# Performance work log

Hardware: AMD Instinct MI355X
Metric: run time of the kernel (lower is better)

Reference implementation:

```python
import jax, jax.numpy as jnp
import numpy as np

B, CIN, COUT = 16, 32, 64
H = W = 64
K = 3                      # kernel side
GRID_SIZE, SPLINE_ORDER = 5, 3
P = K * K                  # in_features of each KANLinear
GR0, GR1 = -1.0, 1.0       # grid_range


def make_grid():
    # torch: grid = arange(-k, G+k+1)*h + grid_range[0], expanded to (in_features, G+2k+1)
    h = (GR1 - GR0) / GRID_SIZE
    g = jnp.arange(-SPLINE_ORDER, GRID_SIZE + SPLINE_ORDER + 1, dtype=jnp.float32) * h + GR0
    return jnp.broadcast_to(g, (P, g.shape[0]))


def b_splines(x, grid):
    # Cox-de Boor recursion. x: (..., P) -> bases: (..., P, GRID_SIZE+SPLINE_ORDER)
    xe = x[..., None]
    bases = ((xe >= grid[:, :-1]) & (xe < grid[:, 1:])).astype(x.dtype)
    for j in range(1, SPLINE_ORDER + 1):
        left = (xe - grid[:, : -(j + 1)]) / (grid[:, j:-1] - grid[:, : -(j + 1)])
        right = (grid[:, j + 1 :] - xe) / (grid[:, j + 1 :] - grid[:, 1:-j])
        bases = left * bases[..., :-1] + right * bases[..., 1:]
    return bases


def setup_inputs() -> dict:
    key = jax.random.key(0)
    k1, k2, k3, k4 = jax.random.split(key, 4)
    x = jax.random.normal(k1, (B, CIN, H, W), dtype=jnp.float32)
    base_weight = jax.random.normal(k2, (COUT, CIN, P), dtype=jnp.float32) * (1.0 / np.sqrt(P))
    spline_weight = jax.random.normal(k3, (COUT, CIN, P, GRID_SIZE + SPLINE_ORDER), dtype=jnp.float32) * 0.1
    spline_scaler = jax.random.normal(k4, (COUT, CIN, P), dtype=jnp.float32) * (1.0 / np.sqrt(P))
    return {"x": x, "base_weight": base_weight, "spline_weight": spline_weight, "spline_scaler": spline_scaler}


def reference(x, base_weight, spline_weight, spline_scaler):
    grid = make_grid()
    # im2col like torch.nn.Unfold: (B, CIN*P, Hout, Wout), channel-major feature order
    patches = jax.lax.conv_general_dilated_patches(x, (K, K), (1, 1), "VALID")
    _, _, Ho, Wo = patches.shape
    patches = patches.reshape(B, CIN, P, Ho * Wo).transpose(0, 1, 3, 2)  # (B, CIN, L, P)
    # base branch: SiLU(x) @ base_weight^T, summed over input channels per output channel
    base_out = jnp.einsum("bclp,ocp->bol", jax.nn.silu(patches), base_weight)
    # spline branch: B-spline bases contracted with scaled spline weights
    bases = b_splines(patches, grid)                       # (B, CIN, L, P, G+k)
    scaled_w = spline_weight * spline_scaler[..., None]    # (COUT, CIN, P, G+k)
    spline_out = jnp.einsum("bclpg,ocpg->bol", bases, scaled_w)
    return (base_out + spline_out).reshape(B, COUT, Ho, Wo)
```

## Files before the change

### kernel.cpp

```cpp
#include <hip/hip_runtime.h>


typedef short v8s __attribute__((ext_vector_type(8)));
typedef float v4f __attribute__((ext_vector_type(4)));
typedef int   v4i __attribute__((ext_vector_type(4)));
typedef int   v8i __attribute__((ext_vector_type(8)));

#define FSPL8_OFF   0u
#define FSILU_OFF   16777472u
#define WMX_OFF     20972032u
#define WF8_OFF     21103104u
#define WPACKS_OFF  21119488u

#define SCALE1 0x7F7F7F7Fu

__device__ __forceinline__ unsigned short f2bf(float f) {
  unsigned int u = __float_as_uint(f);
  u += 0x7fffu + ((u >> 16) & 1u);
  return (unsigned short)(u >> 16);
}

__global__ __launch_bounds__(256) void k_feat(const float* __restrict__ x,
                                              unsigned char* __restrict__ ws) {
  const int bid = blockIdx.x;
  const int b = bid >> 6, y = bid & 63;
  const int t = threadIdx.x;
  const int xx = t & 63, cg = t >> 6;
  unsigned short h[8];
#pragma unroll
  for (int k = 0; k < 8; ++k) {
    const int c = cg * 8 + k;
    const float v = x[(((size_t)(b * 32 + c) * 64 + y) * 64) + xx];
    h[k] = f2bf(v / (1.0f + __expf(-v)));
    float bb[11];
#pragma unroll
    for (int i = 0; i < 11; ++i) {
      float t0 = -2.2f + 0.4f * i;
      bb[i] = (v >= t0 && v < t0 + 0.4f) ? 1.0f : 0.0f;
    }
#pragma unroll
    for (int j = 1; j <= 3; ++j) {
      float rj = 1.0f / (0.4f * j);
#pragma unroll
      for (int i = 0; i + j < 11; ++i) {
        float ti = -2.2f + 0.4f * i;
        bb[i] = (v - ti) * rj * bb[i] + ((ti + 0.4f * (j + 1)) - v) * rj * bb[i + 1];
      }
    }
    uint2 o;
    unsigned w0 = __builtin_amdgcn_cvt_pk_fp8_f32(bb[0], bb[1], 0, false);
    w0 = __builtin_amdgcn_cvt_pk_fp8_f32(bb[2], bb[3], w0, true);
    unsigned w1 = __builtin_amdgcn_cvt_pk_fp8_f32(bb[4], bb[5], 0, false);
    w1 = __builtin_amdgcn_cvt_pk_fp8_f32(bb[6], bb[7], w1, true);
    o.x = w0; o.y = w1;
    *(uint2*)(ws + FSPL8_OFF + ((((size_t)(b * 32 + c) * 64 + y) * 64) + xx) * 8) = o;
  }
  uint4 s;
  s.x = (unsigned)h[0] | ((unsigned)h[1] << 16);
  s.y = (unsigned)h[2] | ((unsigned)h[3] << 16);
  s.z = (unsigned)h[4] | ((unsigned)h[5] << 16);
  s.w = (unsigned)h[6] | ((unsigned)h[7] << 16);
  *(uint4*)(ws + FSILU_OFF + (size_t)(b * 4096 + y * 64 + xx) * 64 + cg * 16) = s;
}

__global__ __launch_bounds__(256) void k_wpack(const float* __restrict__ bw,
                                               const float* __restrict__ sw,
                                               const float* __restrict__ sc,
                                               unsigned char* __restrict__ ws) {
  int tid = blockIdx.x * 256 + threadIdx.x;
  if (tid >= 165888) return;
  if (tid < 147456) {
    int k, dst;
    if (tid < 131072) {
      int bh = tid & 15, lane = (tid >> 4) & 63, pc = (tid >> 10) & 1;
      int ss = (tid >> 13) & 1, p = tid >> 14;
      k = p * 288 + ss * 128 + (lane >> 4) * 32 + pc * 16 + bh;
      dst = WMX_OFF + tid;
    } else {
      int t2 = tid - 131072;
      int e = t2 & 7, lane = (t2 >> 3) & 63, p = t2 >> 11;
      k = p * 288 + 256 + (lane >> 4) * 8 + e;
      dst = WF8_OFF + t2;
    }
    int ot = (tid < 131072) ? ((tid >> 11) & 3) : (((tid - 131072) >> 9) & 3);
    int lane = (tid < 131072) ? ((tid >> 4) & 63) : (((tid - 131072) >> 3) & 63);
    int o = (ot << 4) + (lane & 15);
    int chunk = k / 24, u = k - chunk * 24;
    int dj = u >> 3, g = u & 7;
    int c = chunk / 3, di = chunk - c * 3;
    int p_tap = di * 3 + dj;
    float val = sw[((size_t)(o * 32 + c) * 9 + p_tap) * 8 + g] *
                sc[(size_t)(o * 32 + c) * 9 + p_tap];
    ws[dst] = (unsigned char)(__builtin_amdgcn_cvt_pk_fp8_f32(val, 0.f, 0, false) & 0xff);
  } else {
    int t2 = tid - 147456;
    int e = t2 & 7, lane = (t2 >> 3) & 63, ot = (t2 >> 9) & 3, sp = t2 >> 11;
    int o = (ot << 4) + (lane & 15);
    int cc = ((lane >> 4) << 3) + e;
    float val = bw[(size_t)(o * 32 + cc) * 9 + sp];
    *(unsigned short*)(ws + WPACKS_OFF + (size_t)t2 * 2) = f2bf(val);
  }
}

__device__ __forceinline__ void ld16(unsigned char* ldsp, const unsigned char* gp) {
  __builtin_amdgcn_global_load_lds(
      (const __attribute__((address_space(1))) unsigned int*)gp,
      (__attribute__((address_space(3))) unsigned int*)ldsp, 16, 0, 0);
}

__global__ __launch_bounds__(512) void k_gemm(const unsigned char* __restrict__ ws,
                                              float* __restrict__ out) {
  __shared__ __align__(16) unsigned char wl8[2][18432];
  __shared__ __align__(16) unsigned char fl8[2][12544];
  __shared__ __align__(16) unsigned char wsil[36864];
  __shared__ __align__(16) unsigned char fsil[25088];

  const int blk = blockIdx.x;
  const int b = blk >> 4, ig = blk & 15;
  const int i0 = ig * 4;
  const int tid = threadIdx.x;
  const int wave = tid >> 6, lane = tid & 63;
  const int q = lane >> 4, ln = lane & 15;
  const int r = wave >> 1, oh = wave & 1;
  const int i = i0 + r;

  auto stage_spl = [&](int p, int bi) {
#pragma unroll
    for (int it = 0; it < 4; ++it) {
      const int u = wave + it * 8;
      if (u < 16) {
        ld16(&wl8[bi][u * 1024], ws + WMX_OFF + (size_t)p * 16384 + (size_t)u * 1024 + lane * 16);
      } else if (u < 18) {
        ld16(&wl8[bi][u * 1024], ws + WF8_OFF + (size_t)p * 2048 + (size_t)(u - 16) * 1024 + lane * 16);
      } else if (u < 30) {
        const int v = u - 18;
        const int cp = v / 3, cr = v - cp * 3;
        ld16(&fl8[bi][v * 1024],
             ws + FSPL8_OFF + ((size_t)((b * 32 + p * 4 + cp) * 64 + i0 + cr * 2)) * 512 + lane * 16);
      }
    }
  };

  auto stage_silu = [&]() {
#pragma unroll
    for (int it = 0; it < 8; ++it) {
      const int u = wave + it * 8;
      if (u < 36) {
        ld16(&wsil[u * 1024], ws + WPACKS_OFF + (size_t)u * 1024 + lane * 16);
      } else if (u < 60) {
        const int v = u - 36;
        const int rr = v >> 2, p4 = v & 3;
        const int y = min(i0 + rr, 63);
        ld16(&fsil[v * 1024],
             ws + FSILU_OFF + (size_t)(b * 64 + y) * 4096 +
                 (p4 * 16 + (lane >> 2)) * 64 + ((lane & 3) ^ ((lane >> 2) & 3)) * 16);
      }
    }
  };

  auto offf = [&](int sg, int qq) {
    int rid = 4 * sg + qq;
    int ch = rid / 3, sub = rid - ch * 3;
    int cp = ch / 3, di = ch - cp * 3;
    return cp * 3072 + (r + di) * 512 + (sub + ln) * 8;
  };
  int offA[4], offB[4];
#pragma unroll
  for (int qq = 0; qq < 4; ++qq) { offA[qq] = offf(q, qq); offB[qq] = offf(4 + q, qq); }
  const int off8 = offf(8, q);

  v4f acc[2][4];
#pragma unroll
  for (int a = 0; a < 2; ++a)
#pragma unroll
    for (int c = 0; c < 4; ++c) acc[a][c] = (v4f){0.f, 0.f, 0.f, 0.f};

  stage_silu();
  stage_spl(0, 0);
  __syncthreads();

#pragma unroll 1
  for (int t = 0; t < 8; ++t) {
    if (t < 7) stage_spl(t + 1, (t + 1) & 1);
    const unsigned char* wb = wl8[t & 1];
    const unsigned char* fb = fl8[t & 1];
#pragma unroll
    for (int ss = 0; ss < 2; ++ss) {
      union { v8i v; v4i h[2]; } wf[2];
#pragma unroll
      for (int tt = 0; tt < 2; ++tt) {
        const unsigned char* wp = wb + ss * 8192 + (oh * 2 + tt) * 2048 + lane * 16;
        wf[tt].h[0] = *(const v4i*)(wp);
        wf[tt].h[1] = *(const v4i*)(wp + 1024);
      }
      const int* offs = ss ? offB : offA;
      union { v8i v; long l[4]; } ff[4];
#pragma unroll
      for (int pt = 0; pt < 4; ++pt)
#pragma unroll
        for (int qq = 0; qq < 4; ++qq)
          ff[pt].l[qq] = *(const long*)(fb + offs[qq] + pt * 128);
#pragma unroll
      for (int tt = 0; tt < 2; ++tt)
#pragma unroll
        for (int pt = 0; pt < 4; ++pt)
          acc[tt][pt] = __builtin_amdgcn_mfma_scale_f32_16x16x128_f8f6f4(
              wf[tt].v, ff[pt].v, acc[tt][pt], 0, 0, 0, SCALE1, 0, SCALE1);
    }
    {
      long w8[2], f8[4];
#pragma unroll
      for (int tt = 0; tt < 2; ++tt)
        w8[tt] = *(const long*)(wb + 16384 + (oh * 2 + tt) * 512 + lane * 8);
#pragma unroll
      for (int pt = 0; pt < 4; ++pt)
        f8[pt] = *(const long*)(fb + off8 + pt * 128);
#pragma unroll
      for (int tt = 0; tt < 2; ++tt)
#pragma unroll
        for (int pt = 0; pt < 4; ++pt)
          acc[tt][pt] = __builtin_amdgcn_mfma_f32_16x16x32_fp8_fp8(
              w8[tt], f8[pt], acc[tt][pt], 0, 0, 0);
    }
    __syncthreads();
  }

#pragma unroll
  for (int e = 0; e < 9; ++e) {
    const int di = e / 3, dj = e % 3;
    v8s wb2[2], fb2[4];
#pragma unroll
    for (int tt = 0; tt < 2; ++tt)
      wb2[tt] = *(const v8s*)(&wsil[0] + e * 4096 + (oh * 2 + tt) * 1024 + lane * 16);
    const int xb = dj + ln;
    const int sbase = (r + di) * 4096 + xb * 64 + ((q ^ (xb & 3)) * 16);
#pragma unroll
    for (int pt = 0; pt < 4; ++pt)
      fb2[pt] = *(const v8s*)(&fsil[0] + sbase + pt * 1024);
#pragma unroll
    for (int tt = 0; tt < 2; ++tt)
#pragma unroll
      for (int pt = 0; pt < 4; ++pt)
        acc[tt][pt] = __builtin_amdgcn_mfma_f32_16x16x32_bf16(
            wb2[tt], fb2[pt], acc[tt][pt], 0, 0, 0);
  }

  if (i < 62) {
#pragma unroll
    for (int tt = 0; tt < 2; ++tt)
#pragma unroll
      for (int pt = 0; pt < 4; ++pt) {
        const int j = pt * 16 + ln;
        if (j < 62) {
#pragma unroll
          for (int rr = 0; rr < 4; ++rr) {
            const int o = (oh * 2 + tt) * 16 + q * 4 + rr;
            out[(((size_t)b * 64 + o) * 62 + i) * 62 + j] = acc[tt][pt][rr];
          }
        }
      }
  }
}

extern "C" void kernel_launch(void* const* d_in, const int* in_sizes, int n_in,
                              void* d_out, int out_size, void* d_ws, size_t ws_size,
                              hipStream_t stream) {
  const float* x  = (const float*)d_in[0];
  const float* bw = (const float*)d_in[1];
  const float* sw = (const float*)d_in[2];
  const float* sc = (const float*)d_in[3];
  unsigned char* ws = (unsigned char*)d_ws;
  float* out = (float*)d_out;

  hipLaunchKernelGGL(k_feat,  dim3(1024), dim3(256), 0, stream, x, ws);
  hipLaunchKernelGGL(k_wpack, dim3(648),  dim3(256), 0, stream, bw, sw, sc, ws);
  hipLaunchKernelGGL(k_gemm,  dim3(256),  dim3(512), 0, stream, ws, out);
}
```

Before: 100.2 us.

## Reorder spline GEMM K-dimension by tap with channel-half feature staging

Changes the spline feature layout to row-major per (batch, row, channel-group) blocks of 16 bytes per pixel. The spline GEMM now loops over the 9 kernel taps in two channel halves using only K=128 scaled FP8 MFMAs, and drops the separate K=32 FP8 tail and its weight pack. Six feature rows are staged once per half and reused across taps via shifted addressing, so the staged weights shrink to 8KB per step. This removes the im2col-style duplicated feature loads and the awkward K remainder, at the cost of more loop iterations, extra barriers and a serialized feature reload between the halves.

```diff
diff --git a/kernel.cpp b/kernel.cpp
--- a/kernel.cpp
+++ b/kernel.cpp
@@ -9,7 +9,6 @@
 #define FSPL8_OFF   0u
 #define FSILU_OFF   16777472u
 #define WMX_OFF     20972032u
-#define WF8_OFF     21103104u
 #define WPACKS_OFF  21119488u
 
 #define SCALE1 0x7F7F7F7Fu
@@ -27,6 +26,7 @@
   const int t = threadIdx.x;
   const int xx = t & 63, cg = t >> 6;
   unsigned short h[8];
+  uint2 sp[8];
 #pragma unroll
   for (int k = 0; k < 8; ++k) {
     const int c = cg * 8 + k;
@@ -47,13 +47,19 @@
         bb[i] = (v - ti) * rj * bb[i] + ((ti + 0.4f * (j + 1)) - v) * rj * bb[i + 1];
       }
     }
-    uint2 o;
     unsigned w0 = __builtin_amdgcn_cvt_pk_fp8_f32(bb[0], bb[1], 0, false);
     w0 = __builtin_amdgcn_cvt_pk_fp8_f32(bb[2], bb[3], w0, true);
     unsigned w1 = __builtin_amdgcn_cvt_pk_fp8_f32(bb[4], bb[5], 0, false);
     w1 = __builtin_amdgcn_cvt_pk_fp8_f32(bb[6], bb[7], w1, true);
-    o.x = w0; o.y = w1;
-    *(uint2*)(ws + FSPL8_OFF + ((((size_t)(b * 32 + c) * 64 + y) * 64) + xx) * 8) = o;
+    sp[k].x = w0; sp[k].y = w1;
+  }
+#pragma unroll
+  for (int m = 0; m < 4; ++m) {
+    uint4 v;
+    v.x = sp[2 * m].x;     v.y = sp[2 * m].y;
+    v.z = sp[2 * m + 1].x; v.w = sp[2 * m + 1].y;
+    *(uint4*)(ws + FSPL8_OFF +
+              ((size_t)((b * 64 + y) * 16 + cg * 4 + m)) * 1024 + xx * 16) = v;
   }
   uint4 s;
   s.x = (unsigned)h[0] | ((unsigned)h[1] << 16);
@@ -70,28 +76,16 @@
   int tid = blockIdx.x * 256 + threadIdx.x;
   if (tid >= 165888) return;
   if (tid < 147456) {
-    int k, dst;
-    if (tid < 131072) {
-      int bh = tid & 15, lane = (tid >> 4) & 63, pc = (tid >> 10) & 1;
-      int ss = (tid >> 13) & 1, p = tid >> 14;
-      k = p * 288 + ss * 128 + (lane >> 4) * 32 + pc * 16 + bh;
-      dst = WMX_OFF + tid;
-    } else {
-      int t2 = tid - 131072;
-      int e = t2 & 7, lane = (t2 >> 3) & 63, p = t2 >> 11;
-      k = p * 288 + 256 + (lane >> 4) * 8 + e;
-      dst = WF8_OFF + t2;
-    }
-    int ot = (tid < 131072) ? ((tid >> 11) & 3) : (((tid - 131072) >> 9) & 3);
-    int lane = (tid < 131072) ? ((tid >> 4) & 63) : (((tid - 131072) >> 3) & 63);
+    int hh = tid & 15, lane = (tid >> 4) & 63, u = (tid >> 10) & 7;
+    int ss = (tid >> 13) & 1, tau = tid >> 14;
+    int ot = u >> 1, pc = u & 1, q = lane >> 4;
+    int m = pc * 16 + hh;
+    int c = 16 * ss + 4 * q + (m >> 3), g = m & 7;
     int o = (ot << 4) + (lane & 15);
-    int chunk = k / 24, u = k - chunk * 24;
-    int dj = u >> 3, g = u & 7;
-    int c = chunk / 3, di = chunk - c * 3;
-    int p_tap = di * 3 + dj;
-    float val = sw[((size_t)(o * 32 + c) * 9 + p_tap) * 8 + g] *
-                sc[(size_t)(o * 32 + c) * 9 + p_tap];
-    ws[dst] = (unsigned char)(__builtin_amdgcn_cvt_pk_fp8_f32(val, 0.f, 0, false) & 0xff);
+    float val = sw[((size_t)(o * 32 + c) * 9 + tau) * 8 + g] *
+                sc[(size_t)(o * 32 + c) * 9 + tau];
+    ws[WMX_OFF + tid] =
+        (unsigned char)(__builtin_amdgcn_cvt_pk_fp8_f32(val, 0.f, 0, false) & 0xff);
   } else {
     int t2 = tid - 147456;
     int e = t2 & 7, lane = (t2 >> 3) & 63, ot = (t2 >> 9) & 3, sp = t2 >> 11;
@@ -110,8 +104,8 @@
 
 __global__ __launch_bounds__(512) void k_gemm(const unsigned char* __restrict__ ws,
                                               float* __restrict__ out) {
-  __shared__ __align__(16) unsigned char wl8[2][18432];
-  __shared__ __align__(16) unsigned char fl8[2][12544];
+  __shared__ __align__(16) unsigned char wmx[2][8192];
+  __shared__ __align__(16) unsigned char feat[49664];
   __shared__ __align__(16) unsigned char wsil[36864];
   __shared__ __align__(16) unsigned char fsil[25088];
 
@@ -124,23 +118,18 @@
   const int r = wave >> 1, oh = wave & 1;
   const int i = i0 + r;
 
-  auto stage_spl = [&](int p, int bi) {
-#pragma unroll
-    for (int it = 0; it < 4; ++it) {
-      const int u = wave + it * 8;
-      if (u < 16) {
-        ld16(&wl8[bi][u * 1024], ws + WMX_OFF + (size_t)p * 16384 + (size_t)u * 1024 + lane * 16);
-      } else if (u < 18) {
-        ld16(&wl8[bi][u * 1024], ws + WF8_OFF + (size_t)p * 2048 + (size_t)(u - 16) * 1024 + lane * 16);
-      } else if (u < 30) {
-        const int v = u - 18;
-        const int cp = v / 3, cr = v - cp * 3;
-        ld16(&fl8[bi][v * 1024],
-             ws + FSPL8_OFF + ((size_t)((b * 32 + p * 4 + cp) * 64 + i0 + cr * 2)) * 512 + lane * 16);
-      }
-    }
-  };
-
+  auto stage_w = [&](int tau, int ss, int bi) {
+    ld16(&wmx[bi][wave * 1024],
+         ws + WMX_OFF + (size_t)((tau * 2 + ss) * 8 + wave) * 1024 + lane * 16);
+  };
+  auto stage_feat = [&](int ss) {
+#pragma unroll
+    for (int it = 0; it < 6; ++it) {
+      const int y = min(i0 + it, 63);
+      ld16(&feat[(it * 8 + wave) * 1024],
+           ws + FSPL8_OFF + (size_t)((b * 64 + y) * 16 + 8 * ss + wave) * 1024 + lane * 16);
+    }
+  };
   auto stage_silu = [&]() {
 #pragma unroll
     for (int it = 0; it < 8; ++it) {
@@ -158,73 +147,49 @@
     }
   };
 
-  auto offf = [&](int sg, int qq) {
-    int rid = 4 * sg + qq;
-    int ch = rid / 3, sub = rid - ch * 3;
-    int cp = ch / 3, di = ch - cp * 3;
-    return cp * 3072 + (r + di) * 512 + (sub + ln) * 8;
-  };
-  int offA[4], offB[4];
-#pragma unroll
-  for (int qq = 0; qq < 4; ++qq) { offA[qq] = offf(q, qq); offB[qq] = offf(4 + q, qq); }
-  const int off8 = offf(8, q);
-
   v4f acc[2][4];
 #pragma unroll
   for (int a = 0; a < 2; ++a)
 #pragma unroll
     for (int c = 0; c < 4; ++c) acc[a][c] = (v4f){0.f, 0.f, 0.f, 0.f};
 
+  auto superstep = [&](int tau, int bi) {
+    const int di = tau / 3, dj = tau - 3 * di;
+    union { v8i v; v4i h[2]; } wf[2], ff[4];
+#pragma unroll
+    for (int tt = 0; tt < 2; ++tt)
+#pragma unroll
+      for (int pc = 0; pc < 2; ++pc)
+        wf[tt].h[pc] = *(const v4i*)(&wmx[bi][((oh * 2 + tt) * 2 + pc) * 1024 + lane * 16]);
+#pragma unroll
+    for (int pt = 0; pt < 4; ++pt) {
+      const int xx = ln + dj + 16 * pt;
+#pragma unroll
+      for (int pc = 0; pc < 2; ++pc)
+        ff[pt].h[pc] = *(const v4i*)(&feat[((r + di) * 8 + 2 * q + pc) * 1024 + xx * 16]);
+    }
+#pragma unroll
+    for (int tt = 0; tt < 2; ++tt)
+#pragma unroll
+      for (int pt = 0; pt < 4; ++pt)
+        acc[tt][pt] = __builtin_amdgcn_mfma_scale_f32_16x16x128_f8f6f4(
+            wf[tt].v, ff[pt].v, acc[tt][pt], 0, 0, 0, SCALE1, 0, SCALE1);
+  };
+
+  stage_w(0, 0, 0);
+  stage_feat(0);
   stage_silu();
-  stage_spl(0, 0);
   __syncthreads();
 
 #pragma unroll 1
-  for (int t = 0; t < 8; ++t) {
-    if (t < 7) stage_spl(t + 1, (t + 1) & 1);
-    const unsigned char* wb = wl8[t & 1];
-    const unsigned char* fb = fl8[t & 1];
-#pragma unroll
-    for (int ss = 0; ss < 2; ++ss) {
-      union { v8i v; v4i h[2]; } wf[2];
-#pragma unroll
-      for (int tt = 0; tt < 2; ++tt) {
-        const unsigned char* wp = wb + ss * 8192 + (oh * 2 + tt) * 2048 + lane * 16;
-        wf[tt].h[0] = *(const v4i*)(wp);
-        wf[tt].h[1] = *(const v4i*)(wp + 1024);
-      }
-      const int* offs = ss ? offB : offA;
-      union { v8i v; long l[4]; } ff[4];
-#pragma unroll
-      for (int pt = 0; pt < 4; ++pt)
-#pragma unroll
-        for (int qq = 0; qq < 4; ++qq)
-          ff[pt].l[qq] = *(const long*)(fb + offs[qq] + pt * 128);
-#pragma unroll
-      for (int tt = 0; tt < 2; ++tt)
-#pragma unroll
-        for (int pt = 0; pt < 4; ++pt)
-          acc[tt][pt] = __builtin_amdgcn_mfma_scale_f32_16x16x128_f8f6f4(
-              wf[tt].v, ff[pt].v, acc[tt][pt], 0, 0, 0, SCALE1, 0, SCALE1);
-    }
-    {
-      long w8[2], f8[4];
-#pragma unroll
-      for (int tt = 0; tt < 2; ++tt)
-        w8[tt] = *(const long*)(wb + 16384 + (oh * 2 + tt) * 512 + lane * 8);
-#pragma unroll
-      for (int pt = 0; pt < 4; ++pt)
-        f8[pt] = *(const long*)(fb + off8 + pt * 128);
-#pragma unroll
-      for (int tt = 0; tt < 2; ++tt)
-#pragma unroll
-        for (int pt = 0; pt < 4; ++pt)
-          acc[tt][pt] = __builtin_amdgcn_mfma_f32_16x16x32_fp8_fp8(
-              w8[tt], f8[pt], acc[tt][pt], 0, 0, 0);
-    }
+  for (int t = 0; t < 9; ++t) {
+    if (t < 8) stage_w(t + 1, 0, (t + 1) & 1);
+    superstep(t, t & 1);
     __syncthreads();
   }
 
+  stage_feat(1);
+  stage_w(0, 1, 1);
 #pragma unroll
   for (int e = 0; e < 9; ++e) {
     const int di = e / 3, dj = e % 3;
@@ -243,6 +208,14 @@
       for (int pt = 0; pt < 4; ++pt)
         acc[tt][pt] = __builtin_amdgcn_mfma_f32_16x16x32_bf16(
             wb2[tt], fb2[pt], acc[tt][pt], 0, 0, 0);
+  }
+  __syncthreads();
+
+#pragma unroll 1
+  for (int t = 0; t < 9; ++t) {
+    if (t < 8) stage_w(t + 1, 1, t & 1);
+    superstep(t, (t + 1) & 1);
+    __syncthreads();
   }
 
   if (i < 62) {
```

Result: no change. 100.4 us (+0.2%).
